# Performance work log

Measured on AMD Instinct MI355X. Metric: run time of the kernel, lower is better.

Reference implementation:

```python
import jax, jax.numpy as jnp
import numpy as np

DIM = 512
HEADS = 1
DIM_HEAD = DIM // 8          # 64
M = DIM // 2                 # 256 landmarks
ITERS = 6                    # pinv iterations
SCALE = DIM_HEAD ** -0.5
KSIZE = 33                   # residual conv kernel (seq dim)
EPS_LN = 1e-5


def setup_inputs() -> dict:
    key = jax.random.key(0)
    ks = jax.random.split(key, 6)
    B, N = 4, 4096  # N multiple of M -> no padding branch
    return {
        "x": jax.random.normal(ks[0], (B, N, DIM), jnp.float32),
        "norm_gamma": jnp.ones((DIM,), jnp.float32),
        "norm_beta": jnp.zeros((DIM,), jnp.float32),
        "w_qkv": jax.random.normal(ks[1], (DIM, 3 * HEADS * DIM_HEAD), jnp.float32) * 0.02,
        "w_out": jax.random.normal(ks[2], (HEADS * DIM_HEAD, DIM), jnp.float32) * 0.02,
        "b_out": jnp.zeros((DIM,), jnp.float32),
        "w_conv": jax.random.normal(ks[3], (HEADS, 1, KSIZE, 1), jnp.float32) * 0.02,
    }


def _moore_penrose_pinv(x, iters=ITERS):
    # x: [B, H, M, M]
    abs_x = jnp.abs(x)
    col = abs_x.sum(-1)
    row = abs_x.sum(-2)
    z = jnp.swapaxes(x, -1, -2) / (jnp.max(col) * jnp.max(row))  # global maxes, as in torch
    I = jnp.eye(x.shape[-1], dtype=x.dtype)
    for _ in range(iters):
        xz = x @ z
        z = 0.25 * z @ (13.0 * I - xz @ (15.0 * I - xz @ (7.0 * I - xz)))
    return z


def reference(x, norm_gamma, norm_beta, w_qkv, w_out, b_out, w_conv):
    B, N, _ = x.shape
    # LayerNorm (biased variance, matches torch)
    mu = x.mean(-1, keepdims=True)
    var = x.var(-1, keepdims=True)
    xn = (x - mu) / jnp.sqrt(var + EPS_LN) * norm_gamma + norm_beta

    qkv = xn @ w_qkv  # [B, N, 3*H*D]
    q, k, v = jnp.split(qkv, 3, axis=-1)
    resh = lambda t: t.reshape(B, N, HEADS, DIM_HEAD).transpose(0, 2, 1, 3)  # [B,H,N,D]
    q, k, v = resh(q), resh(k), resh(v)
    q = q * SCALE

    # landmarks: mean of l=N/M consecutive tokens
    l = N // M
    q_l = q.reshape(B, HEADS, M, l, DIM_HEAD).sum(3) / l  # [B,H,M,D]
    k_l = k.reshape(B, HEADS, M, l, DIM_HEAD).sum(3) / l

    sim1 = jnp.einsum('bhnd,bhmd->bhnm', q, k_l)    # [B,H,N,M]
    sim2 = jnp.einsum('bhid,bhjd->bhij', q_l, k_l)  # [B,H,M,M]
    sim3 = jnp.einsum('bhmd,bhnd->bhmn', q_l, k)    # [B,H,M,N]
    a1 = jax.nn.softmax(sim1, axis=-1)
    a2 = jax.nn.softmax(sim2, axis=-1)
    a3 = jax.nn.softmax(sim3, axis=-1)

    a2_inv = _moore_penrose_pinv(a2)
    left = a1 @ a2_inv                      # [B,H,N,M]
    out = left @ (a3 @ v)                   # [B,H,N,D]

    # residual depthwise conv over the sequence dim (treat [N,D] as HxW image)
    res = jax.lax.conv_general_dilated(
        v, w_conv, window_strides=(1, 1),
        padding=((KSIZE // 2, KSIZE // 2), (0, 0)),
        dimension_numbers=('NCHW', 'OIHW', 'NCHW'),
        feature_group_count=HEADS)
    out = out + res

    out = out.transpose(0, 2, 1, 3).reshape(B, N, HEADS * DIM_HEAD)
    out = out @ w_out + b_out               # to_out (dropout is eval no-op)

    attn = left @ a3                        # full approx attention [B,H,N,N]
    return (x + out, attn)
```

## Files before the change

kernel.cpp:

```cpp
#include <hip/hip_runtime.h>
#include <hip/hip_bf16.h>


typedef _Float16 f16;
typedef f16 f16x2 __attribute__((ext_vector_type(2)));
typedef f16 f16x4 __attribute__((ext_vector_type(4)));
typedef f16 f16x8 __attribute__((ext_vector_type(8)));
typedef float f32x4 __attribute__((ext_vector_type(4)));

__device__ __forceinline__ float waveMax(float v){
  #pragma unroll
  for(int i=32;i>0;i>>=1) v = fmaxf(v, __shfl_xor(v, i));
  return v;
}
__device__ __forceinline__ float waveSum(float v){
  #pragma unroll
  for(int i=32;i>0;i>>=1) v += __shfl_xor(v, i);
  return v;
}
__device__ __forceinline__ float blockMaxF(float v, float* sm){
  v = waveMax(v);
  if((threadIdx.x&63)==0) sm[threadIdx.x>>6] = v;
  __syncthreads();
  v = fmaxf(fmaxf(sm[0],sm[1]), fmaxf(sm[2],sm[3]));
  __syncthreads();
  return v;
}
__device__ __forceinline__ float blockSumF(float v, float* sm){
  v = waveSum(v);
  if((threadIdx.x&63)==0) sm[threadIdx.x>>6] = v;
  __syncthreads();
  v = sm[0]+sm[1]+sm[2]+sm[3];
  __syncthreads();
  return v;
}

__device__ __forceinline__ void st_out(float* p, float v){ *p = v; }
__device__ __forceinline__ void st_out(f16* p, float v){ *p = (f16)v; }

__device__ __forceinline__ void async_cp16(const f16* g, const f16* l){
  __builtin_amdgcn_global_load_lds((const __attribute__((address_space(1))) void*)g,
                                   (__attribute__((address_space(3))) void*)l, 16, 0, 0);
}

__global__ __launch_bounds__(256) void k_ln(const float* __restrict__ x, const float* __restrict__ g,
                                            const float* __restrict__ be, f16* __restrict__ xn){
  __shared__ float sm[8];
  long row = blockIdx.x; int t = threadIdx.x;
  const float* xr = x + row*512;
  float v0 = xr[t], v1 = xr[t+256];
  float s = waveSum(v0+v1), ss = waveSum(v0*v0+v1*v1);
  if((t&63)==0){ sm[t>>6] = s; sm[(t>>6)+4] = ss; }
  __syncthreads();
  s = sm[0]+sm[1]+sm[2]+sm[3]; ss = sm[4]+sm[5]+sm[6]+sm[7];
  float mu = s*(1.f/512.f);
  float var = ss*(1.f/512.f) - mu*mu;
  float rstd = rsqrtf(var + 1e-5f);
  xn[row*512+t]     = (f16)((v0-mu)*rstd*g[t]     + be[t]);
  xn[row*512+t+256] = (f16)((v1-mu)*rstd*g[t+256] + be[t+256]);
}

__global__ __launch_bounds__(256) void k_prep(const float* __restrict__ wqkv, const float* __restrict__ wout,
    f16* __restrict__ wqkT, f16* __restrict__ woutT, float* __restrict__ rs, unsigned* __restrict__ csmax){
  int blk = blockIdx.x, t = threadIdx.x;
  if(blk < 512){
    int i = blk*256 + t; int n = i>>9, k = i&511;
    wqkT[i] = (n<192) ? (f16)wqkv[k*192+n] : (f16)0.0f;
  } else if(blk < 640){
    int i = (blk-512)*256 + t; int n = i>>6, k = i&63;
    woutT[i] = (f16)wout[k*512+n];
  } else {
    rs[t]=0.f; rs[t+256]=0.f; rs[t+512]=0.f; rs[t+768]=0.f;
    if(t==0) *csmax = 0u;
  }
}

template<typename OutT>
__global__ __launch_bounds__(256) void gemm_bt(
    const f16* __restrict__ A, const f16* __restrict__ Bt, OutT* __restrict__ C,
    int M, int N, int K, long sA, long sB, long sC, int kbeg, int kend, int kslog,
    long sSlice, const float* __restrict__ bias, const float* __restrict__ resid)
{
  __shared__ f16 As[8192];
  __shared__ f16 Bs[8192];
  int zz = blockIdx.z;
  int b  = zz >> kslog;
  int ksl = zz & ((1<<kslog)-1);
  A  += (long)b * sA;  Bt += (long)b * sB;  C += (long)b * sC + (long)ksl * sSlice;
  int m0 = blockIdx.x*128, n0 = blockIdx.y*128;
  int t = threadIdx.x;
  int w = t>>6, lane = t&63;
  int quad = lane>>4, l16 = lane&15;
  int wr = w>>1, wc = w&1;
  int tiles = (kend - kbeg) >> 6;
  int per = tiles >> kslog;
  int kt0 = (kbeg>>6) + ksl*per;
  f32x4 acc[4][4] = {};
  for(int kt=kt0; kt<kt0+per; ++kt){
    #pragma unroll
    for(int i=0;i<4;++i){
      int G = (w<<8)+(i<<6)+lane;
      int row = G>>3, gs = G&7;
      int g = gs ^ (row&7);
      int koff = (kt<<6)+(g<<3);
      const f16* ldst = As + (((w<<8)+(i<<6))<<3);
      async_cp16(A + (long)(m0+row)*K + koff, ldst);
      const f16* ldst2 = Bs + (((w<<8)+(i<<6))<<3);
      async_cp16(Bt + (long)(n0+row)*K + koff, ldst2);
    }
    __syncthreads();
    #pragma unroll
    for(int kk=0; kk<2; ++kk){
      f16x8 af[4], bfr[4];
      int gb = (kk<<2) + quad;
      #pragma unroll
      for(int mi=0;mi<4;++mi){
        int row = (wr<<6)+(mi<<4)+l16;
        af[mi] = *(const f16x8*)(As + ((row<<6) + ((gb ^ (row&7))<<3)));
      }
      #pragma unroll
      for(int ni=0;ni<4;++ni){
        int row = (wc<<6)+(ni<<4)+l16;
        bfr[ni] = *(const f16x8*)(Bs + ((row<<6) + ((gb ^ (row&7))<<3)));
      }
      #pragma unroll
      for(int mi=0;mi<4;++mi){
        #pragma unroll
        for(int ni=0;ni<4;++ni)
          acc[mi][ni] = __builtin_amdgcn_mfma_f32_16x16x32_f16(af[mi], bfr[ni], acc[mi][ni], 0,0,0);
      }
    }
    __syncthreads();
  }
  #pragma unroll
  for(int mi=0;mi<4;++mi){
    int rowb = m0 + (wr<<6) + (mi<<4) + (quad<<2);
    #pragma unroll
    for(int ni=0;ni<4;++ni){
      int col = n0 + (wc<<6) + (ni<<4) + l16;
      if(col < N){
        #pragma unroll
        for(int r=0;r<4;++r){
          float v = acc[mi][ni][r];
          if(bias)  v += bias[col];
          if(resid) v += resid[(long)(rowb+r)*N + col];
          st_out(C + (long)(rowb+r)*N + col, v);
        }
      }
    }
  }
}

__global__ __launch_bounds__(256) void k_split(const float* __restrict__ qkv,
    f16* __restrict__ qf, f16* __restrict__ kf, float* __restrict__ vf){
  int t = threadIdx.x;
  long row = (long)blockIdx.x*4 + (t>>6); int d = t&63;
  const float* p = qkv + row*192;
  qf[row*64+d] = (f16)(p[d]*0.125f);
  kf[row*64+d] = (f16)(p[d+64]);
  vf[row*64+d] = p[d+128];
}

__global__ __launch_bounds__(256) void k_vT(const float* __restrict__ vf, f16* __restrict__ vT){
  __shared__ float tile[64][65];
  int b = blockIdx.y, n0 = blockIdx.x*64;
  int t = threadIdx.x; int c = t&63, r4 = t>>6;
  #pragma unroll
  for(int i=0;i<16;++i){ int r = i*4+r4; tile[r][c] = vf[((long)(b*4096 + n0 + r))*64 + c]; }
  __syncthreads();
  #pragma unroll
  for(int i=0;i<16;++i){ int d = i*4+r4;
    vT[((long)(b*128 + d))*4096 + n0 + c] = (f16)tile[c][d]; }
}

__global__ __launch_bounds__(256) void k_land(const f16* __restrict__ qf, const f16* __restrict__ kf,
                                              f16* __restrict__ ql, f16* __restrict__ kl){
  int t = threadIdx.x;
  int bm = blockIdx.x*4 + (t>>6); int d = t&63;
  const f16* pq = qf + (long)bm*1024 + d;
  const f16* pk = kf + (long)bm*1024 + d;
  float sq=0.f, sk=0.f;
  #pragma unroll
  for(int i=0;i<16;++i){ sq += (float)pq[i*64]; sk += (float)pk[i*64]; }
  ql[bm*64+d] = (f16)(sq*0.0625f);
  kl[bm*64+d] = (f16)(sk*0.0625f);
}

__global__ __launch_bounds__(256) void k_softmax1(const float* __restrict__ s, f16* __restrict__ a){
  int t = threadIdx.x; int w = t>>6, lane = t&63;
  long row = (long)blockIdx.x*4 + w;
  float4 v = *(const float4*)(s + row*256 + lane*4);
  float m = waveMax(fmaxf(fmaxf(v.x,v.y),fmaxf(v.z,v.w)));
  float e0 = __expf(v.x-m), e1 = __expf(v.y-m), e2 = __expf(v.z-m), e3 = __expf(v.w-m);
  float inv = 1.f/waveSum(e0+e1+e2+e3);
  f16x4 o = {(f16)(e0*inv),(f16)(e1*inv),(f16)(e2*inv),(f16)(e3*inv)};
  *(f16x4*)(a + row*256 + lane*4) = o;
}

__global__ __launch_bounds__(256) void k_softmax2(const float* __restrict__ s, float* __restrict__ a2,
                                                  float* __restrict__ rs, unsigned* __restrict__ csmax){
  __shared__ float sm[4];
  int row = blockIdx.x; int t = threadIdx.x; int b = row>>8;
  float v = s[row*256+t];
  float m = blockMaxF(v, sm);
  float e = __expf(v-m);
  float sum = blockSumF(e, sm);
  float p = e/sum;
  a2[(long)row*256+t] = p;
  atomicAdd(&rs[b*256+t], p);
  float rowsum = blockSumF(p, sm);
  if(t==0) atomicMax(csmax, __float_as_uint(rowsum));
}

__global__ __launch_bounds__(256) void k_softmax3(const float* __restrict__ s, f16* __restrict__ a){
  __shared__ float sm[4];
  long row = blockIdx.x; int t = threadIdx.x;
  const float* p = s + row*4096;
  float4 v[4]; float m = -1e30f;
  #pragma unroll
  for(int i=0;i<4;++i){
    v[i] = *(const float4*)(p + (i*256+t)*4);
    m = fmaxf(m, fmaxf(fmaxf(v[i].x,v[i].y),fmaxf(v[i].z,v[i].w)));
  }
  m = blockMaxF(m, sm);
  float sum = 0.f;
  #pragma unroll
  for(int i=0;i<4;++i){
    v[i].x = __expf(v[i].x-m); v[i].y = __expf(v[i].y-m);
    v[i].z = __expf(v[i].z-m); v[i].w = __expf(v[i].w-m);
    sum += v[i].x+v[i].y+v[i].z+v[i].w;
  }
  float inv = 1.f/blockSumF(sum, sm);
  f16* o = a + row*4096;
  #pragma unroll
  for(int i=0;i<4;++i){
    f16x4 ov = {(f16)(v[i].x*inv),(f16)(v[i].y*inv),(f16)(v[i].z*inv),(f16)(v[i].w*inv)};
    *(f16x4*)(o + (i*256+t)*4) = ov;
  }
}

__global__ __launch_bounds__(256) void k_z0(const float* __restrict__ a2, const float* __restrict__ rs,
                                            const unsigned* __restrict__ csmax, float* __restrict__ z){
  __shared__ float tile[64][65];
  __shared__ float sm[4];
  int b = blockIdx.z; int i0 = blockIdx.x*64, j0 = blockIdx.y*64;
  int t = threadIdx.x;
  float m = fmaxf(fmaxf(rs[t],rs[t+256]), fmaxf(rs[t+512],rs[t+768]));
  m = blockMaxF(m, sm);
  float sc = 1.f/(__uint_as_float(*csmax)*m);
  const float* A = a2 + (long)b*65536; float* Z = z + (long)b*65536;
  int c = t&63, r4 = t>>6;
  #pragma unroll
  for(int i=0;i<16;++i){ int r = i*4+r4; tile[r][c] = A[(j0+r)*256 + i0 + c]; }
  __syncthreads();
  #pragma unroll
  for(int i=0;i<16;++i){ int r = i*4+r4; Z[(i0+r)*256 + j0 + c] = tile[c][r]*sc; }
}

template<int AS, int BS, int ES>
__global__ __launch_bounds__(256) void gemm256s(const float* __restrict__ A, const float* __restrict__ B,
    const float* __restrict__ E, float* __restrict__ D, int Ncols, float beta, float alpha){
  __shared__ float At[16][72];
  __shared__ float Bs[16][72];
  int z = blockIdx.z; int b = z&3, ks = z>>2;
  long aOff = (long)b*65536;
  long bBatch = 256L*Ncols, bSl = 4L*bBatch;
  long bOff = (long)b*bBatch;
  long dOff = (long)ks*bSl + bOff;
  int r0 = blockIdx.x*64, c0 = blockIdx.y*64;
  int t = threadIdx.x, tr = t>>4, tc = t&15;
  int arow = t>>2, ac4 = t&3;
  int bk = t>>4, bn4 = t&15;
  float acc[4][4] = {};
  for(int k0=ks*64;k0<ks*64+64;k0+=16){
    const float* pa = A + aOff + (long)(r0+arow)*256 + k0 + ac4*4;
    float4 va = *(const float4*)pa;
    #pragma unroll
    for(int s=1;s<AS;++s){ float4 w = *(const float4*)(pa + (long)s*262144);
      va.x+=w.x; va.y+=w.y; va.z+=w.z; va.w+=w.w; }
    At[ac4*4+0][arow]=va.x; At[ac4*4+1][arow]=va.y; At[ac4*4+2][arow]=va.z; At[ac4*4+3][arow]=va.w;
    const float* pb = B + bOff + (long)(k0+bk)*Ncols + c0 + bn4*4;
    float4 vb = *(const float4*)pb;
    #pragma unroll
    for(int s=1;s<BS;++s){ float4 w = *(const float4*)(pb + (long)s*bSl);
      vb.x+=w.x; vb.y+=w.y; vb.z+=w.z; vb.w+=w.w; }
    *(float4*)&Bs[bk][bn4*4] = vb;
    __syncthreads();
    #pragma unroll
    for(int kk=0;kk<16;++kk){
      float4 a4 = *(const float4*)&At[kk][tr*4];
      float4 b4 = *(const float4*)&Bs[kk][tc*4];
      float av[4] = {a4.x,a4.y,a4.z,a4.w};
      float bv[4] = {b4.x,b4.y,b4.z,b4.w};
      #pragma unroll
      for(int i=0;i<4;++i){
        #pragma unroll
        for(int j=0;j<4;++j) acc[i][j] += av[i]*bv[j];
      }
    }
    __syncthreads();
  }
  #pragma unroll
  for(int i=0;i<4;++i){
    int row = r0 + tr*4 + i;
    #pragma unroll
    for(int j=0;j<4;++j){
      int col = c0 + tc*4 + j;
      float v = beta*acc[i][j];
      if(ES>0 && ks==0){
        const float* pe = E + aOff + (long)row*256 + col;
        float e = pe[0];
        #pragma unroll
        for(int s=1;s<ES;++s) e += pe[(long)s*262144];
        v += alpha*e;
      }
      D[dOff + (long)row*Ncols + col] = v;
    }
  }
}

__global__ __launch_bounds__(256) void k_zb(const float* __restrict__ z, f16* __restrict__ zb){
  int i = blockIdx.x*256 + threadIdx.x;
  float v = z[i] + z[i+262144] + z[i+524288] + z[i+786432];
  zb[i] = (f16)v;
}

__global__ __launch_bounds__(256) void k_trA3(const f16* __restrict__ a3, f16* __restrict__ a3T){
  __shared__ f16 tile[64][74];
  int b = blockIdx.z; int n0 = blockIdx.x*64, m0 = blockIdx.y*64;
  const f16* A = a3 + (long)b*1048576; f16* T = a3T + (long)b*1048576;
  int t = threadIdx.x; int c = t&63, r4 = t>>6;
  #pragma unroll
  for(int i=0;i<16;++i){ int r = i*4+r4; tile[r][c] = A[(long)(m0+r)*4096 + n0 + c]; }
  __syncthreads();
  #pragma unroll
  for(int i=0;i<16;++i){ int nr = i*4+r4; T[(long)(n0+nr)*256 + m0 + c] = tile[c][nr]; }
}

__global__ __launch_bounds__(256) void k_trZ(const float* __restrict__ pW, f16* __restrict__ zaT){
  int i = blockIdx.x*256 + threadIdx.x;
  int b = i>>15, j = i&32767; int d = j>>8, m = j&255;
  float v = 0.f;
  if(d<64){
    long base = (long)b*16384 + (long)m*64 + d;
    v = pW[base] + pW[base+65536] + pW[base+131072] + pW[base+196608];
  }
  zaT[i] = (f16)v;
}

__global__ __launch_bounds__(256) void k_h(const float* __restrict__ outh, const float* __restrict__ vf,
                                           const float* __restrict__ wconv, f16* __restrict__ h){
  __shared__ float wc[33];
  if(threadIdx.x<33) wc[threadIdx.x]=wconv[threadIdx.x];
  __syncthreads();
  long e = (long)blockIdx.x*256 + threadIdx.x;
  int d = (int)(e&63); long row = e>>6; int n = (int)(row&4095); long brow = row - n;
  float acc = outh[e];
  #pragma unroll
  for(int tau=0;tau<33;++tau){
    int nn = n + tau - 16;
    if(nn>=0 && nn<4096) acc += wc[tau]*vf[(brow+nn)*64 + d];
  }
  h[e] = (f16)acc;
}

extern "C" void kernel_launch(void* const* d_in, const int* in_sizes, int n_in,
                              void* d_out, int out_size, void* d_ws, size_t ws_size,
                              hipStream_t stream) {
  (void)in_sizes; (void)n_in; (void)out_size; (void)ws_size;
  const float* x     = (const float*)d_in[0];
  const float* gamma = (const float*)d_in[1];
  const float* beta  = (const float*)d_in[2];
  const float* wqkv  = (const float*)d_in[3];
  const float* wout  = (const float*)d_in[4];
  const float* bout  = (const float*)d_in[5];
  const float* wconv = (const float*)d_in[6];

  char* ws = (char*)d_ws;
  f16*   xn   = (f16*)(ws + 0);
  float* s3   = (float*)(ws + 0);
  float* s1   = (float*)(ws + 16777216);
  f16*   a3T  = (f16*)(ws + 16777216);
  f16*   U    = (f16*)(ws + 25165824);
  float* qkv  = (float*)(ws + 33554432);
  f16*   a3   = (f16*)(ws + 33554432);
  f16*   a1   = (f16*)(ws + 46137344);
  f16*   qf   = (f16*)(ws + 54525952);
  f16*   kf   = (f16*)(ws + 56623104);
  float* vf   = (float*)(ws + 58720256);
  f16*   vT   = (f16*)(ws + 62914560);
  f16*   wqkT = (f16*)(ws + 67108864);
  f16*   ql   = (f16*)(ws + 67371008);
  f16*   kl   = (f16*)(ws + 67502080);
  float* s2   = (float*)(ws + 67633152);
  float* a2   = (float*)(ws + 68681728);
  float* zA   = (float*)(ws + 69730304);
  f16*   zb   = (f16*)(ws + 74973184);
  float* rs   = (float*)(ws + 76021760);
  unsigned* csmax = (unsigned*)(ws + 76021760 + 4096);
  f16*   zaT  = (f16*)(ws + 76029952);
  f16*   woutT= (f16*)(ws + 76292096);
  float* outh = (float*)(ws + 76357632);
  f16*   h    = (f16*)(ws + 80551936);
  float* pXZ  = (float*)(ws + 82649088);
  float* pT1  = (float*)(ws + 86843392);
  float* pT2  = (float*)(ws + 91037696);
  float* pU0  = (float*)(ws + 95232000);
  float* pU1  = (float*)(ws + 99426304);
  float* a3vp = (float*)(ws + 103620608);
  float* pW   = (float*)(ws + 105717760);

  float* out0 = (float*)d_out;
  float* attn = out0 + 8388608;

  k_prep<<<641,256,0,stream>>>(wqkv, wout, wqkT, woutT, rs, csmax);
  k_ln<<<16384,256,0,stream>>>(x, gamma, beta, xn);
  gemm_bt<float><<<dim3(128,2,1),256,0,stream>>>(xn, wqkT, qkv, 16384,192,512, 0L,0L,0L, 0,512,0, 0L, nullptr,nullptr);
  k_split<<<4096,256,0,stream>>>(qkv, qf, kf, vf);
  k_vT<<<dim3(64,4),256,0,stream>>>(vf, vT);
  k_land<<<256,256,0,stream>>>(qf, kf, ql, kl);
  gemm_bt<float><<<dim3(32,2,4),256,0,stream>>>(qf, kl, s1, 4096,256,64, 262144L,16384L,1048576L, 0,64,0, 0L, nullptr,nullptr);
  gemm_bt<float><<<dim3(2,2,4),256,0,stream>>>(ql, kl, s2, 256,256,64, 16384L,16384L,65536L, 0,64,0, 0L, nullptr,nullptr);
  gemm_bt<float><<<dim3(2,32,4),256,0,stream>>>(ql, kf, s3, 256,4096,64, 16384L,262144L,1048576L, 0,64,0, 0L, nullptr,nullptr);
  k_softmax1<<<4096,256,0,stream>>>(s1, a1);
  k_softmax2<<<1024,256,0,stream>>>(s2, a2, rs, csmax);
  k_softmax3<<<1024,256,0,stream>>>(s3, a3);
  k_z0<<<dim3(4,4,4),256,0,stream>>>(a2, rs, csmax, zA);
  {
    float* cur = zA;
    float* bufs[2] = {pU0, pU1};
    for(int it=0; it<6; ++it){
      float* nxt = bufs[it&1];
      if(it==0) gemm256s<1,1,0><<<dim3(4,4,16),256,0,stream>>>(a2, cur, nullptr, pXZ, 256, 1.f, 0.f);
      else      gemm256s<1,4,0><<<dim3(4,4,16),256,0,stream>>>(a2, cur, nullptr, pXZ, 256, 1.f, 0.f);
      gemm256s<4,4,4><<<dim3(4,4,16),256,0,stream>>>(pXZ, pXZ, pXZ, pT1, 256, -1.f, 7.f);
      gemm256s<4,4,4><<<dim3(4,4,16),256,0,stream>>>(pXZ, pT1, pXZ, pT2, 256, -1.f, 15.f);
      if(it==0) gemm256s<1,4,1><<<dim3(4,4,16),256,0,stream>>>(cur, pT2, cur, nxt, 256, -0.25f, 3.25f);
      else      gemm256s<4,4,4><<<dim3(4,4,16),256,0,stream>>>(cur, pT2, cur, nxt, 256, -0.25f, 3.25f);
      cur = nxt;
    }
    k_zb<<<1024,256,0,stream>>>(cur, zb);
    k_trA3<<<dim3(64,4,4),256,0,stream>>>(a3, a3T);
    gemm_bt<float><<<dim3(2,1,32),256,0,stream>>>(a3, vT, a3vp, 256,64,4096, 1048576L,524288L,16384L, 0,4096,3, 65536L, nullptr,nullptr);
    gemm256s<4,8,0><<<dim3(4,1,16),256,0,stream>>>(cur, a3vp, nullptr, pW, 64, 1.f, 0.f);
  }
  k_trZ<<<512,256,0,stream>>>(pW, zaT);
  gemm_bt<float><<<dim3(32,1,4),256,0,stream>>>(a1, zaT, outh, 4096,64,256, 1048576L,32768L,262144L, 0,256,0, 0L, nullptr,nullptr);
  k_h<<<4096,256,0,stream>>>(outh, vf, wconv, h);
  gemm_bt<float><<<dim3(128,4,1),256,0,stream>>>(h, woutT, out0, 16384,512,64, 0L,0L,0L, 0,64,0, 0L, bout, x);
  gemm_bt<f16><<<dim3(32,2,4),256,0,stream>>>(a3T, zb, U, 4096,256,256, 1048576L,65536L,1048576L, 0,256,0, 0L, nullptr,nullptr);
  gemm_bt<float><<<dim3(32,32,4),256,0,stream>>>(a1, U, attn, 4096,4096,256, 1048576L,1048576L,16777216L, 0,256,0, 0L, nullptr,nullptr);
}
```

Measured before the change: 834.0 us.

## Merge independent stages into fused launches and run pinv loop in persistent kernel

Independent kernels are merged into multi-role launches that dispatch on block index: LN with weight prep, split with vT and landmarks, the three sim GEMMs, the three softmaxes, the outh and U GEMMs, and the out-projection with the attn GEMM. The 24 Newton-Schulz pinv GEMM launches plus z0, zb and trZ become one persistent 256-block kernel that uses a global atomic grid barrier between steps. The aim is to cut launch count and tail idle time between small kernels. The grid barrier assumes all 256 blocks are co-resident, and a spin-wait costs something of its own.

Result: slower. 1.389 ms (+66.5%).

```diff
diff --git a/kernel.cpp b/kernel.cpp
--- a/kernel.cpp
+++ b/kernel.cpp
@@ -35,78 +35,45 @@
   return v;
 }
 
-__device__ __forceinline__ void st_out(float* p, float v){ *p = v; }
-__device__ __forceinline__ void st_out(f16* p, float v){ *p = (f16)v; }
-
 __device__ __forceinline__ void async_cp16(const f16* g, const f16* l){
   __builtin_amdgcn_global_load_lds((const __attribute__((address_space(1))) void*)g,
                                    (__attribute__((address_space(3))) void*)l, 16, 0, 0);
 }
 
-__global__ __launch_bounds__(256) void k_ln(const float* __restrict__ x, const float* __restrict__ g,
-                                            const float* __restrict__ be, f16* __restrict__ xn){
-  __shared__ float sm[8];
-  long row = blockIdx.x; int t = threadIdx.x;
-  const float* xr = x + row*512;
-  float v0 = xr[t], v1 = xr[t+256];
-  float s = waveSum(v0+v1), ss = waveSum(v0*v0+v1*v1);
-  if((t&63)==0){ sm[t>>6] = s; sm[(t>>6)+4] = ss; }
-  __syncthreads();
-  s = sm[0]+sm[1]+sm[2]+sm[3]; ss = sm[4]+sm[5]+sm[6]+sm[7];
-  float mu = s*(1.f/512.f);
-  float var = ss*(1.f/512.f) - mu*mu;
-  float rstd = rsqrtf(var + 1e-5f);
-  xn[row*512+t]     = (f16)((v0-mu)*rstd*g[t]     + be[t]);
-  xn[row*512+t+256] = (f16)((v1-mu)*rstd*g[t+256] + be[t+256]);
-}
-
-__global__ __launch_bounds__(256) void k_prep(const float* __restrict__ wqkv, const float* __restrict__ wout,
-    f16* __restrict__ wqkT, f16* __restrict__ woutT, float* __restrict__ rs, unsigned* __restrict__ csmax){
-  int blk = blockIdx.x, t = threadIdx.x;
-  if(blk < 512){
-    int i = blk*256 + t; int n = i>>9, k = i&511;
-    wqkT[i] = (n<192) ? (f16)wqkv[k*192+n] : (f16)0.0f;
-  } else if(blk < 640){
-    int i = (blk-512)*256 + t; int n = i>>6, k = i&63;
-    woutT[i] = (f16)wout[k*512+n];
-  } else {
-    rs[t]=0.f; rs[t+256]=0.f; rs[t+512]=0.f; rs[t+768]=0.f;
-    if(t==0) *csmax = 0u;
-  }
-}
-
-template<typename OutT>
-__global__ __launch_bounds__(256) void gemm_bt(
-    const f16* __restrict__ A, const f16* __restrict__ Bt, OutT* __restrict__ C,
-    int M, int N, int K, long sA, long sB, long sC, int kbeg, int kend, int kslog,
-    long sSlice, const float* __restrict__ bias, const float* __restrict__ resid)
+__device__ __forceinline__ void gridBar(unsigned* bar, unsigned* s, int nb){
+  __syncthreads();
+  if(threadIdx.x==0){
+    __builtin_amdgcn_fence(__ATOMIC_RELEASE, "agent");
+    __hip_atomic_fetch_add(bar, 1u, __ATOMIC_RELAXED, __HIP_MEMORY_SCOPE_AGENT);
+    unsigned target = (unsigned)nb * (*s + 1u);
+    while(__hip_atomic_load(bar, __ATOMIC_RELAXED, __HIP_MEMORY_SCOPE_AGENT) < target)
+      __builtin_amdgcn_s_sleep(2);
+    __builtin_amdgcn_fence(__ATOMIC_ACQUIRE, "agent");
+  }
+  ++*s;
+  __syncthreads();
+}
+
+__device__ __forceinline__ void gemm_body(
+    const f16* __restrict__ A, const f16* __restrict__ Bt, void* __restrict__ C, int cf16,
+    int N, int K, int m0, int n0, int kt0, int ktn,
+    const float* __restrict__ bias, const float* __restrict__ resid,
+    f16* As, f16* Bs)
 {
-  __shared__ f16 As[8192];
-  __shared__ f16 Bs[8192];
-  int zz = blockIdx.z;
-  int b  = zz >> kslog;
-  int ksl = zz & ((1<<kslog)-1);
-  A  += (long)b * sA;  Bt += (long)b * sB;  C += (long)b * sC + (long)ksl * sSlice;
-  int m0 = blockIdx.x*128, n0 = blockIdx.y*128;
   int t = threadIdx.x;
   int w = t>>6, lane = t&63;
   int quad = lane>>4, l16 = lane&15;
   int wr = w>>1, wc = w&1;
-  int tiles = (kend - kbeg) >> 6;
-  int per = tiles >> kslog;
-  int kt0 = (kbeg>>6) + ksl*per;
   f32x4 acc[4][4] = {};
-  for(int kt=kt0; kt<kt0+per; ++kt){
+  for(int kt=kt0; kt<kt0+ktn; ++kt){
     #pragma unroll
     for(int i=0;i<4;++i){
       int G = (w<<8)+(i<<6)+lane;
       int row = G>>3, gs = G&7;
       int g = gs ^ (row&7);
       int koff = (kt<<6)+(g<<3);
-      const f16* ldst = As + (((w<<8)+(i<<6))<<3);
-      async_cp16(A + (long)(m0+row)*K + koff, ldst);
-      const f16* ldst2 = Bs + (((w<<8)+(i<<6))<<3);
-      async_cp16(Bt + (long)(n0+row)*K + koff, ldst2);
+      async_cp16(A + (long)(m0+row)*K + koff, As + (((w<<8)+(i<<6))<<3));
+      async_cp16(Bt + (long)(n0+row)*K + koff, Bs + (((w<<8)+(i<<6))<<3));
     }
     __syncthreads();
     #pragma unroll
@@ -144,130 +111,23 @@
           float v = acc[mi][ni][r];
           if(bias)  v += bias[col];
           if(resid) v += resid[(long)(rowb+r)*N + col];
-          st_out(C + (long)(rowb+r)*N + col, v);
+          if(cf16) ((f16*)C)[(long)(rowb+r)*N + col] = (f16)v;
+          else     ((float*)C)[(long)(rowb+r)*N + col] = v;
         }
       }
     }
   }
 }
 
-__global__ __launch_bounds__(256) void k_split(const float* __restrict__ qkv,
-    f16* __restrict__ qf, f16* __restrict__ kf, float* __restrict__ vf){
-  int t = threadIdx.x;
-  long row = (long)blockIdx.x*4 + (t>>6); int d = t&63;
-  const float* p = qkv + row*192;
-  qf[row*64+d] = (f16)(p[d]*0.125f);
-  kf[row*64+d] = (f16)(p[d+64]);
-  vf[row*64+d] = p[d+128];
-}
-
-__global__ __launch_bounds__(256) void k_vT(const float* __restrict__ vf, f16* __restrict__ vT){
-  __shared__ float tile[64][65];
-  int b = blockIdx.y, n0 = blockIdx.x*64;
-  int t = threadIdx.x; int c = t&63, r4 = t>>6;
-  #pragma unroll
-  for(int i=0;i<16;++i){ int r = i*4+r4; tile[r][c] = vf[((long)(b*4096 + n0 + r))*64 + c]; }
-  __syncthreads();
-  #pragma unroll
-  for(int i=0;i<16;++i){ int d = i*4+r4;
-    vT[((long)(b*128 + d))*4096 + n0 + c] = (f16)tile[c][d]; }
-}
-
-__global__ __launch_bounds__(256) void k_land(const f16* __restrict__ qf, const f16* __restrict__ kf,
-                                              f16* __restrict__ ql, f16* __restrict__ kl){
-  int t = threadIdx.x;
-  int bm = blockIdx.x*4 + (t>>6); int d = t&63;
-  const f16* pq = qf + (long)bm*1024 + d;
-  const f16* pk = kf + (long)bm*1024 + d;
-  float sq=0.f, sk=0.f;
-  #pragma unroll
-  for(int i=0;i<16;++i){ sq += (float)pq[i*64]; sk += (float)pk[i*64]; }
-  ql[bm*64+d] = (f16)(sq*0.0625f);
-  kl[bm*64+d] = (f16)(sk*0.0625f);
-}
-
-__global__ __launch_bounds__(256) void k_softmax1(const float* __restrict__ s, f16* __restrict__ a){
-  int t = threadIdx.x; int w = t>>6, lane = t&63;
-  long row = (long)blockIdx.x*4 + w;
-  float4 v = *(const float4*)(s + row*256 + lane*4);
-  float m = waveMax(fmaxf(fmaxf(v.x,v.y),fmaxf(v.z,v.w)));
-  float e0 = __expf(v.x-m), e1 = __expf(v.y-m), e2 = __expf(v.z-m), e3 = __expf(v.w-m);
-  float inv = 1.f/waveSum(e0+e1+e2+e3);
-  f16x4 o = {(f16)(e0*inv),(f16)(e1*inv),(f16)(e2*inv),(f16)(e3*inv)};
-  *(f16x4*)(a + row*256 + lane*4) = o;
-}
-
-__global__ __launch_bounds__(256) void k_softmax2(const float* __restrict__ s, float* __restrict__ a2,
-                                                  float* __restrict__ rs, unsigned* __restrict__ csmax){
-  __shared__ float sm[4];
-  int row = blockIdx.x; int t = threadIdx.x; int b = row>>8;
-  float v = s[row*256+t];
-  float m = blockMaxF(v, sm);
-  float e = __expf(v-m);
-  float sum = blockSumF(e, sm);
-  float p = e/sum;
-  a2[(long)row*256+t] = p;
-  atomicAdd(&rs[b*256+t], p);
-  float rowsum = blockSumF(p, sm);
-  if(t==0) atomicMax(csmax, __float_as_uint(rowsum));
-}
-
-__global__ __launch_bounds__(256) void k_softmax3(const float* __restrict__ s, f16* __restrict__ a){
-  __shared__ float sm[4];
-  long row = blockIdx.x; int t = threadIdx.x;
-  const float* p = s + row*4096;
-  float4 v[4]; float m = -1e30f;
-  #pragma unroll
-  for(int i=0;i<4;++i){
-    v[i] = *(const float4*)(p + (i*256+t)*4);
-    m = fmaxf(m, fmaxf(fmaxf(v[i].x,v[i].y),fmaxf(v[i].z,v[i].w)));
-  }
-  m = blockMaxF(m, sm);
-  float sum = 0.f;
-  #pragma unroll
-  for(int i=0;i<4;++i){
-    v[i].x = __expf(v[i].x-m); v[i].y = __expf(v[i].y-m);
-    v[i].z = __expf(v[i].z-m); v[i].w = __expf(v[i].w-m);
-    sum += v[i].x+v[i].y+v[i].z+v[i].w;
-  }
-  float inv = 1.f/blockSumF(sum, sm);
-  f16* o = a + row*4096;
-  #pragma unroll
-  for(int i=0;i<4;++i){
-    f16x4 ov = {(f16)(v[i].x*inv),(f16)(v[i].y*inv),(f16)(v[i].z*inv),(f16)(v[i].w*inv)};
-    *(f16x4*)(o + (i*256+t)*4) = ov;
-  }
-}
-
-__global__ __launch_bounds__(256) void k_z0(const float* __restrict__ a2, const float* __restrict__ rs,
-                                            const unsigned* __restrict__ csmax, float* __restrict__ z){
-  __shared__ float tile[64][65];
-  __shared__ float sm[4];
-  int b = blockIdx.z; int i0 = blockIdx.x*64, j0 = blockIdx.y*64;
-  int t = threadIdx.x;
-  float m = fmaxf(fmaxf(rs[t],rs[t+256]), fmaxf(rs[t+512],rs[t+768]));
-  m = blockMaxF(m, sm);
-  float sc = 1.f/(__uint_as_float(*csmax)*m);
-  const float* A = a2 + (long)b*65536; float* Z = z + (long)b*65536;
-  int c = t&63, r4 = t>>6;
-  #pragma unroll
-  for(int i=0;i<16;++i){ int r = i*4+r4; tile[r][c] = A[(j0+r)*256 + i0 + c]; }
-  __syncthreads();
-  #pragma unroll
-  for(int i=0;i<16;++i){ int r = i*4+r4; Z[(i0+r)*256 + j0 + c] = tile[c][r]*sc; }
-}
-
-template<int AS, int BS, int ES>
-__global__ __launch_bounds__(256) void gemm256s(const float* __restrict__ A, const float* __restrict__ B,
-    const float* __restrict__ E, float* __restrict__ D, int Ncols, float beta, float alpha){
-  __shared__ float At[16][72];
-  __shared__ float Bs[16][72];
-  int z = blockIdx.z; int b = z&3, ks = z>>2;
+__device__ __forceinline__ void g256_body(const float* __restrict__ A, const float* __restrict__ B,
+    const float* __restrict__ E, float* __restrict__ D, int Ncols, float beta, float alpha,
+    int AS, int BS, int ES, int bx, int by, int b, int ks, float* At, float* Bss)
+{
   long aOff = (long)b*65536;
   long bBatch = 256L*Ncols, bSl = 4L*bBatch;
   long bOff = (long)b*bBatch;
   long dOff = (long)ks*bSl + bOff;
-  int r0 = blockIdx.x*64, c0 = blockIdx.y*64;
+  int r0 = bx*64, c0 = by*64;
   int t = threadIdx.x, tr = t>>4, tc = t&15;
   int arow = t>>2, ac4 = t&3;
   int bk = t>>4, bn4 = t&15;
@@ -275,21 +135,20 @@
   for(int k0=ks*64;k0<ks*64+64;k0+=16){
     const float* pa = A + aOff + (long)(r0+arow)*256 + k0 + ac4*4;
     float4 va = *(const float4*)pa;
-    #pragma unroll
-    for(int s=1;s<AS;++s){ float4 w = *(const float4*)(pa + (long)s*262144);
-      va.x+=w.x; va.y+=w.y; va.z+=w.z; va.w+=w.w; }
-    At[ac4*4+0][arow]=va.x; At[ac4*4+1][arow]=va.y; At[ac4*4+2][arow]=va.z; At[ac4*4+3][arow]=va.w;
+    for(int s=1;s<AS;++s){ float4 w2 = *(const float4*)(pa + (long)s*262144);
+      va.x+=w2.x; va.y+=w2.y; va.z+=w2.z; va.w+=w2.w; }
+    At[(ac4*4+0)*72+arow]=va.x; At[(ac4*4+1)*72+arow]=va.y;
+    At[(ac4*4+2)*72+arow]=va.z; At[(ac4*4+3)*72+arow]=va.w;
     const float* pb = B + bOff + (long)(k0+bk)*Ncols + c0 + bn4*4;
     float4 vb = *(const float4*)pb;
-    #pragma unroll
-    for(int s=1;s<BS;++s){ float4 w = *(const float4*)(pb + (long)s*bSl);
-      vb.x+=w.x; vb.y+=w.y; vb.z+=w.z; vb.w+=w.w; }
-    *(float4*)&Bs[bk][bn4*4] = vb;
+    for(int s=1;s<BS;++s){ float4 w2 = *(const float4*)(pb + (long)s*bSl);
+      vb.x+=w2.x; vb.y+=w2.y; vb.z+=w2.z; vb.w+=w2.w; }
+    *(float4*)&Bss[bk*72+bn4*4] = vb;
     __syncthreads();
     #pragma unroll
     for(int kk=0;kk<16;++kk){
-      float4 a4 = *(const float4*)&At[kk][tr*4];
-      float4 b4 = *(const float4*)&Bs[kk][tc*4];
+      float4 a4 = *(const float4*)&At[kk*72+tr*4];
+      float4 b4 = *(const float4*)&Bss[kk*72+tc*4];
       float av[4] = {a4.x,a4.y,a4.z,a4.w};
       float bv[4] = {b4.x,b4.y,b4.z,b4.w};
       #pragma unroll
@@ -310,7 +169,6 @@
       if(ES>0 && ks==0){
         const float* pe = E + aOff + (long)row*256 + col;
         float e = pe[0];
-        #pragma unroll
         for(int s=1;s<ES;++s) e += pe[(long)s*262144];
         v += alpha*e;
       }
@@ -319,33 +177,263 @@
   }
 }
 
-__global__ __launch_bounds__(256) void k_zb(const float* __restrict__ z, f16* __restrict__ zb){
-  int i = blockIdx.x*256 + threadIdx.x;
-  float v = z[i] + z[i+262144] + z[i+524288] + z[i+786432];
-  zb[i] = (f16)v;
-}
-
-__global__ __launch_bounds__(256) void k_trA3(const f16* __restrict__ a3, f16* __restrict__ a3T){
+__global__ __launch_bounds__(256) void k_ln_prep(const float* __restrict__ x, const float* __restrict__ g,
+    const float* __restrict__ be, f16* __restrict__ xn, const float* __restrict__ wqkv,
+    const float* __restrict__ wout, f16* __restrict__ wqkT, f16* __restrict__ woutT,
+    float* __restrict__ rs, unsigned* __restrict__ csmax, unsigned* __restrict__ bar){
+  __shared__ float sm[8];
+  int blk = blockIdx.x; int t = threadIdx.x;
+  if(blk < 16384){
+    long row = blk;
+    const float* xr = x + row*512;
+    float v0 = xr[t], v1 = xr[t+256];
+    float s = waveSum(v0+v1), ss = waveSum(v0*v0+v1*v1);
+    if((t&63)==0){ sm[t>>6] = s; sm[(t>>6)+4] = ss; }
+    __syncthreads();
+    s = sm[0]+sm[1]+sm[2]+sm[3]; ss = sm[4]+sm[5]+sm[6]+sm[7];
+    float mu = s*(1.f/512.f);
+    float var = ss*(1.f/512.f) - mu*mu;
+    float rstd = rsqrtf(var + 1e-5f);
+    xn[row*512+t]     = (f16)((v0-mu)*rstd*g[t]     + be[t]);
+    xn[row*512+t+256] = (f16)((v1-mu)*rstd*g[t+256] + be[t+256]);
+  } else if(blk < 16896){
+    int i = (blk-16384)*256 + t; int n = i>>9, k = i&511;
+    wqkT[i] = (n<192) ? (f16)wqkv[k*192+n] : (f16)0.0f;
+  } else if(blk < 17024){
+    int i = (blk-16896)*256 + t; int n = i>>6, k = i&63;
+    woutT[i] = (f16)wout[k*512+n];
+  } else {
+    rs[t]=0.f; rs[t+256]=0.f; rs[t+512]=0.f; rs[t+768]=0.f;
+    if(t==0){ *csmax = 0u; *bar = 0u; }
+  }
+}
+
+__global__ __launch_bounds__(256) void k_qkv(const f16* __restrict__ xn, const f16* __restrict__ wqkT,
+                                             float* __restrict__ qkv){
+  __shared__ f16 As[8192];
+  __shared__ f16 Bs[8192];
+  int blk = blockIdx.x;
+  int bx = blk&127, by = blk>>7;
+  gemm_body(xn, wqkT, qkv, 0, 192, 512, bx*128, by*128, 0, 8, nullptr, nullptr, As, Bs);
+}
+
+__global__ __launch_bounds__(256) void k_splitvl(const float* __restrict__ qkv,
+    f16* __restrict__ qf, f16* __restrict__ kf, float* __restrict__ vf,
+    f16* __restrict__ vT, f16* __restrict__ ql, f16* __restrict__ kl){
+  __shared__ float tile[64][65];
+  int blk = blockIdx.x; int t = threadIdx.x;
+  if(blk < 4096){
+    long row = (long)blk*4 + (t>>6); int d = t&63;
+    const float* p = qkv + row*192;
+    qf[row*64+d] = (f16)(p[d]*0.125f);
+    kf[row*64+d] = (f16)(p[d+64]);
+    vf[row*64+d] = p[d+128];
+  } else if(blk < 4352){
+    int bidx = blk-4096; int b = bidx>>6, n0 = (bidx&63)*64;
+    int c = t&63, r4 = t>>6;
+    #pragma unroll
+    for(int i=0;i<16;++i){ int r = i*4+r4;
+      tile[r][c] = qkv[((long)(b*4096 + n0 + r))*192 + 128 + c]; }
+    __syncthreads();
+    #pragma unroll
+    for(int i=0;i<16;++i){ int d = i*4+r4;
+      vT[((long)(b*128 + d))*4096 + n0 + c] = (f16)tile[c][d]; }
+  } else {
+    int bidx = blk-4352;
+    int bm = bidx*4 + (t>>6); int d = t&63;
+    const float* p = qkv + (long)bm*16*192;
+    float sq=0.f, sk=0.f;
+    #pragma unroll
+    for(int i=0;i<16;++i){ sq += p[i*192+d]; sk += p[i*192+64+d]; }
+    ql[bm*64+d] = (f16)(sq*0.0625f*0.125f);
+    kl[bm*64+d] = (f16)(sk*0.0625f);
+  }
+}
+
+__global__ __launch_bounds__(256) void k_sims(const f16* __restrict__ qf, const f16* __restrict__ kf,
+    const f16* __restrict__ ql, const f16* __restrict__ kl,
+    float* __restrict__ s1, float* __restrict__ s2, float* __restrict__ s3){
+  __shared__ f16 As[8192];
+  __shared__ f16 Bs[8192];
+  int blk = blockIdx.x;
+  if(blk < 256){
+    int bx = blk&31, by = (blk>>5)&1, b = blk>>6;
+    gemm_body(qf + (long)b*262144, kl + (long)b*16384, s1 + (long)b*1048576, 0,
+              256, 64, bx*128, by*128, 0, 1, nullptr, nullptr, As, Bs);
+  } else if(blk < 272){
+    int idx = blk-256;
+    int bx = idx&1, by = (idx>>1)&1, b = idx>>2;
+    gemm_body(ql + (long)b*16384, kl + (long)b*16384, s2 + (long)b*65536, 0,
+              256, 64, bx*128, by*128, 0, 1, nullptr, nullptr, As, Bs);
+  } else {
+    int idx = blk-272;
+    int bx = idx&1, by = (idx>>1)&31, b = idx>>6;
+    gemm_body(ql + (long)b*16384, kf + (long)b*262144, s3 + (long)b*1048576, 0,
+              4096, 64, bx*128, by*128, 0, 1, nullptr, nullptr, As, Bs);
+  }
+}
+
+__global__ __launch_bounds__(256) void k_softmaxes(const float* __restrict__ s1, f16* __restrict__ a1,
+    const float* __restrict__ s2, float* __restrict__ a2, float* __restrict__ rs, unsigned* __restrict__ csmax,
+    const float* __restrict__ s3, f16* __restrict__ a3){
+  __shared__ float sm[4];
+  int blk = blockIdx.x; int t = threadIdx.x;
+  if(blk < 4096){
+    int w = t>>6, lane = t&63;
+    long row = (long)blk*4 + w;
+    float4 v = *(const float4*)(s1 + row*256 + lane*4);
+    float m = waveMax(fmaxf(fmaxf(v.x,v.y),fmaxf(v.z,v.w)));
+    float e0 = __expf(v.x-m), e1 = __expf(v.y-m), e2 = __expf(v.z-m), e3 = __expf(v.w-m);
+    float inv = 1.f/waveSum(e0+e1+e2+e3);
+    f16x4 o = {(f16)(e0*inv),(f16)(e1*inv),(f16)(e2*inv),(f16)(e3*inv)};
+    *(f16x4*)(a1 + row*256 + lane*4) = o;
+  } else if(blk < 5120){
+    int row = blk-4096; int b = row>>8;
+    float v = s2[row*256+t];
+    float m = blockMaxF(v, sm);
+    float e = __expf(v-m);
+    float sum = blockSumF(e, sm);
+    float p = e/sum;
+    a2[(long)row*256+t] = p;
+    atomicAdd(&rs[b*256+t], p);
+    float rowsum = blockSumF(p, sm);
+    if(t==0) atomicMax(csmax, __float_as_uint(rowsum));
+  } else {
+    long row = blk-5120;
+    const float* p = s3 + row*4096;
+    float4 v[4]; float m = -1e30f;
+    #pragma unroll
+    for(int i=0;i<4;++i){
+      v[i] = *(const float4*)(p + (i*256+t)*4);
+      m = fmaxf(m, fmaxf(fmaxf(v[i].x,v[i].y),fmaxf(v[i].z,v[i].w)));
+    }
+    m = blockMaxF(m, sm);
+    float sum = 0.f;
+    #pragma unroll
+    for(int i=0;i<4;++i){
+      v[i].x = __expf(v[i].x-m); v[i].y = __expf(v[i].y-m);
+      v[i].z = __expf(v[i].z-m); v[i].w = __expf(v[i].w-m);
+      sum += v[i].x+v[i].y+v[i].z+v[i].w;
+    }
+    float inv = 1.f/blockSumF(sum, sm);
+    f16* o = a3 + row*4096;
+    #pragma unroll
+    for(int i=0;i<4;++i){
+      f16x4 ov = {(f16)(v[i].x*inv),(f16)(v[i].y*inv),(f16)(v[i].z*inv),(f16)(v[i].w*inv)};
+      *(f16x4*)(o + (i*256+t)*4) = ov;
+    }
+  }
+}
+
+__global__ __launch_bounds__(256) void k_trA3_a3v(const f16* __restrict__ a3, f16* __restrict__ a3T,
+    const f16* __restrict__ vT, float* __restrict__ a3vp){
+  __shared__ f16 As[8192];
+  __shared__ f16 Bs[8192];
   __shared__ f16 tile[64][74];
-  int b = blockIdx.z; int n0 = blockIdx.x*64, m0 = blockIdx.y*64;
-  const f16* A = a3 + (long)b*1048576; f16* T = a3T + (long)b*1048576;
-  int t = threadIdx.x; int c = t&63, r4 = t>>6;
+  int blk = blockIdx.x; int t = threadIdx.x;
+  if(blk < 1024){
+    int bx = blk&63, by = (blk>>6)&3, b = blk>>8;
+    int n0 = bx*64, m0 = by*64;
+    const f16* A = a3 + (long)b*1048576; f16* T = a3T + (long)b*1048576;
+    int c = t&63, r4 = t>>6;
+    #pragma unroll
+    for(int i=0;i<16;++i){ int r = i*4+r4; tile[r][c] = A[(long)(m0+r)*4096 + n0 + c]; }
+    __syncthreads();
+    #pragma unroll
+    for(int i=0;i<16;++i){ int nr = i*4+r4; T[(long)(n0+nr)*256 + m0 + c] = tile[c][nr]; }
+  } else {
+    int idx = blk-1024;
+    int bx = idx&1, zz = idx>>1;
+    int b = zz>>3, ksl = zz&7;
+    gemm_body(a3 + (long)b*1048576, vT + (long)b*524288,
+              a3vp + (long)ksl*65536 + (long)b*16384, 0,
+              64, 4096, bx*128, 0, ksl*8, 8, nullptr, nullptr, As, Bs);
+  }
+}
+
+__global__ __launch_bounds__(256) void k_pinv(const float* __restrict__ a2, const float* __restrict__ rs,
+    const unsigned* __restrict__ csmax, float* __restrict__ zA,
+    float* __restrict__ pXZ, float* __restrict__ pT1, float* __restrict__ pT2,
+    float* __restrict__ pU0, float* __restrict__ pU1,
+    const float* __restrict__ a3vp, float* __restrict__ pW,
+    f16* __restrict__ zb, f16* __restrict__ zaT, unsigned* __restrict__ bar)
+{
+  __shared__ float smem[4164];
+  int blk = blockIdx.x; int t = threadIdx.x;
+  unsigned s = 0;
+  if(blk < 64){
+    int ix = blk&3, jy = (blk>>2)&3, b = blk>>4;
+    int i0 = ix*64, j0 = jy*64;
+    float m = fmaxf(fmaxf(rs[t],rs[t+256]), fmaxf(rs[t+512],rs[t+768]));
+    m = blockMaxF(m, smem+4160);
+    float sc = 1.f/(__uint_as_float(*csmax)*m);
+    const float* A = a2 + (long)b*65536; float* Z = zA + (long)b*65536;
+    int c = t&63, r4 = t>>6;
+    #pragma unroll
+    for(int i=0;i<16;++i){ int r = i*4+r4; smem[r*65+c] = A[(j0+r)*256 + i0 + c]; }
+    __syncthreads();
+    #pragma unroll
+    for(int i=0;i<16;++i){ int r = i*4+r4; Z[(i0+r)*256 + j0 + c] = smem[c*65+r]*sc; }
+  }
+  gridBar(bar, &s, 256);
+  int bx = blk&3, by = (blk>>2)&3, b4 = (blk>>4)&3, ks = blk>>6;
+  float* At = smem; float* Bss = smem+1152;
+  const float* cur = zA; int curAS = 1;
+  float* bufs[2] = {pU0, pU1};
+  for(int it=0; it<6; ++it){
+    float* nxt = bufs[it&1];
+    g256_body(a2, cur, nullptr, pXZ, 256, 1.f, 0.f, 1, curAS, 0, bx,by,b4,ks, At,Bss);
+    gridBar(bar, &s, 256);
+    g256_body(pXZ, pXZ, pXZ, pT1, 256, -1.f, 7.f, 4,4,4, bx,by,b4,ks, At,Bss);
+    gridBar(bar, &s, 256);
+    g256_body(pXZ, pT1, pXZ, pT2, 256, -1.f, 15.f, 4,4,4, bx,by,b4,ks, At,Bss);
+    gridBar(bar, &s, 256);
+    g256_body(cur, pT2, cur, nxt, 256, -0.25f, 3.25f, curAS,4,curAS, bx,by,b4,ks, At,Bss);
+    gridBar(bar, &s, 256);
+    cur = nxt; curAS = 4;
+  }
+  if(blk < 64){
+    int zx = blk&3, zz = blk>>2;
+    int zb4 = zz&3, zks = zz>>2;
+    g256_body(cur, a3vp, nullptr, pW, 64, 1.f, 0.f, 4,8,0, zx,0,zb4,zks, At,Bss);
+  } else if(blk < 192){
+    int base = (blk-64)*2048;
+    #pragma unroll
+    for(int k=0;k<8;++k){
+      int i = base + k*256 + t;
+      float v = cur[i] + cur[i+262144] + cur[i+524288] + cur[i+786432];
+      zb[i] = (f16)v;
+    }
+  }
+  gridBar(bar, &s, 256);
   #pragma unroll
-  for(int i=0;i<16;++i){ int r = i*4+r4; tile[r][c] = A[(long)(m0+r)*4096 + n0 + c]; }
-  __syncthreads();
-  #pragma unroll
-  for(int i=0;i<16;++i){ int nr = i*4+r4; T[(long)(n0+nr)*256 + m0 + c] = tile[c][nr]; }
-}
-
-__global__ __launch_bounds__(256) void k_trZ(const float* __restrict__ pW, f16* __restrict__ zaT){
-  int i = blockIdx.x*256 + threadIdx.x;
-  int b = i>>15, j = i&32767; int d = j>>8, m = j&255;
-  float v = 0.f;
-  if(d<64){
-    long base = (long)b*16384 + (long)m*64 + d;
-    v = pW[base] + pW[base+65536] + pW[base+131072] + pW[base+196608];
-  }
-  zaT[i] = (f16)v;
+  for(int j=0;j<2;++j){
+    int i = blk*512 + j*256 + t;
+    int b = i>>15, j2 = i&32767; int d = j2>>8, m = j2&255;
+    float v = 0.f;
+    if(d<64){
+      long base = (long)b*16384 + (long)m*64 + d;
+      v = pW[base] + pW[base+65536] + pW[base+131072] + pW[base+196608];
+    }
+    zaT[i] = (f16)v;
+  }
+}
+
+__global__ __launch_bounds__(256) void k_outh_U(const f16* __restrict__ a1, const f16* __restrict__ zaT,
+    float* __restrict__ outh, const f16* __restrict__ a3T, const f16* __restrict__ zb, f16* __restrict__ U){
+  __shared__ f16 As[8192];
+  __shared__ f16 Bs[8192];
+  int blk = blockIdx.x;
+  if(blk < 128){
+    int bx = blk&31, b = blk>>5;
+    gemm_body(a1 + (long)b*1048576, zaT + (long)b*32768, outh + (long)b*262144, 0,
+              64, 256, bx*128, 0, 0, 4, nullptr, nullptr, As, Bs);
+  } else {
+    int idx = blk-128;
+    int bx = idx&31, by = (idx>>5)&1, b = idx>>6;
+    gemm_body(a3T + (long)b*1048576, zb + (long)b*65536, U + (long)b*1048576, 1,
+              256, 256, bx*128, by*128, 0, 4, nullptr, nullptr, As, Bs);
+  }
 }
 
 __global__ __launch_bounds__(256) void k_h(const float* __restrict__ outh, const float* __restrict__ vf,
@@ -362,6 +450,23 @@
     if(nn>=0 && nn<4096) acc += wc[tau]*vf[(brow+nn)*64 + d];
   }
   h[e] = (f16)acc;
+}
+
+__global__ __launch_bounds__(256) void k_out_attn(const f16* __restrict__ h, const f16* __restrict__ woutT,
+    const float* __restrict__ x, const float* __restrict__ bout, float* __restrict__ out0,
+    const f16* __restrict__ a1, const f16* __restrict__ U, float* __restrict__ attn){
+  __shared__ f16 As[8192];
+  __shared__ f16 Bs[8192];
+  int blk = blockIdx.x;
+  if(blk < 512){
+    int bx = blk&127, by = blk>>7;
+    gemm_body(h, woutT, out0, 0, 512, 64, bx*128, by*128, 0, 1, bout, x, As, Bs);
+  } else {
+    int idx = blk-512;
+    int bx = idx&31, by = (idx>>5)&31, b = idx>>10;
+    gemm_body(a1 + (long)b*1048576, U + (long)b*1048576, attn + (long)b*16777216, 0,
+              4096, 256, bx*128, by*128, 0, 4, nullptr, nullptr, As, Bs);
+  }
 }
 
 extern "C" void kernel_launch(void* const* d_in, const int* in_sizes, int n_in,
@@ -398,6 +503,7 @@
   f16*   zb   = (f16*)(ws + 74973184);
   float* rs   = (float*)(ws + 76021760);
   unsigned* csmax = (unsigned*)(ws + 76021760 + 4096);
+  unsigned* bar   = (unsigned*)(ws + 76021760 + 4160);
   f16*   zaT  = (f16*)(ws + 76029952);
   f16*   woutT= (f16*)(ws + 76292096);
   float* outh = (float*)(ws + 76357632);
@@ -413,41 +519,14 @@
   float* out0 = (float*)d_out;
   float* attn = out0 + 8388608;
 
-  k_prep<<<641,256,0,stream>>>(wqkv, wout, wqkT, woutT, rs, csmax);
-  k_ln<<<16384,256,0,stream>>>(x, gamma, beta, xn);
-  gemm_bt<float><<<dim3(128,2,1),256,0,stream>>>(xn, wqkT, qkv, 16384,192,512, 0L,0L,0L, 0,512,0, 0L, nullptr,nullptr);
-  k_split<<<4096,256,0,stream>>>(qkv, qf, kf, vf);
-  k_vT<<<dim3(64,4),256,0,stream>>>(vf, vT);
-  k_land<<<256,256,0,stream>>>(qf, kf, ql, kl);
-  gemm_bt<float><<<dim3(32,2,4),256,0,stream>>>(qf, kl, s1, 4096,256,64, 262144L,16384L,1048576L, 0,64,0, 0L, nullptr,nullptr);
-  gemm_bt<float><<<dim3(2,2,4),256,0,stream>>>(ql, kl, s2, 256,256,64, 16384L,16384L,65536L, 0,64,0, 0L, nullptr,nullptr);
-  gemm_bt<float><<<dim3(2,32,4),256,0,stream>>>(ql, kf, s3, 256,4096,64, 16384L,262144L,1048576L, 0,64,0, 0L, nullptr,nullptr);
-  k_softmax1<<<4096,256,0,stream>>>(s1, a1);
-  k_softmax2<<<1024,256,0,stream>>>(s2, a2, rs, csmax);
-  k_softmax3<<<1024,256,0,stream>>>(s3, a3);
-  k_z0<<<dim3(4,4,4),256,0,stream>>>(a2, rs, csmax, zA);
-  {
-    float* cur = zA;
-    float* bufs[2] = {pU0, pU1};
-    for(int it=0; it<6; ++it){
-      float* nxt = bufs[it&1];
-      if(it==0) gemm256s<1,1,0><<<dim3(4,4,16),256,0,stream>>>(a2, cur, nullptr, pXZ, 256, 1.f, 0.f);
-      else      gemm256s<1,4,0><<<dim3(4,4,16),256,0,stream>>>(a2, cur, nullptr, pXZ, 256, 1.f, 0.f);
-      gemm256s<4,4,4><<<dim3(4,4,16),256,0,stream>>>(pXZ, pXZ, pXZ, pT1, 256, -1.f, 7.f);
-      gemm256s<4,4,4><<<dim3(4,4,16),256,0,stream>>>(pXZ, pT1, pXZ, pT2, 256, -1.f, 15.f);
-      if(it==0) gemm256s<1,4,1><<<dim3(4,4,16),256,0,stream>>>(cur, pT2, cur, nxt, 256, -0.25f, 3.25f);
-      else      gemm256s<4,4,4><<<dim3(4,4,16),256,0,stream>>>(cur, pT2, cur, nxt, 256, -0.25f, 3.25f);
-      cur = nxt;
-    }
-    k_zb<<<1024,256,0,stream>>>(cur, zb);
-    k_trA3<<<dim3(64,4,4),256,0,stream>>>(a3, a3T);
-    gemm_bt<float><<<dim3(2,1,32),256,0,stream>>>(a3, vT, a3vp, 256,64,4096, 1048576L,524288L,16384L, 0,4096,3, 65536L, nullptr,nullptr);
-    gemm256s<4,8,0><<<dim3(4,1,16),256,0,stream>>>(cur, a3vp, nullptr, pW, 64, 1.f, 0.f);
-  }
-  k_trZ<<<512,256,0,stream>>>(pW, zaT);
-  gemm_bt<float><<<dim3(32,1,4),256,0,stream>>>(a1, zaT, outh, 4096,64,256, 1048576L,32768L,262144L, 0,256,0, 0L, nullptr,nullptr);
+  k_ln_prep<<<17025,256,0,stream>>>(x, gamma, beta, xn, wqkv, wout, wqkT, woutT, rs, csmax, bar);
+  k_qkv<<<256,256,0,stream>>>(xn, wqkT, qkv);
+  k_splitvl<<<4608,256,0,stream>>>(qkv, qf, kf, vf, vT, ql, kl);
+  k_sims<<<528,256,0,stream>>>(qf, kf, ql, kl, s1, s2, s3);
+  k_softmaxes<<<6144,256,0,stream>>>(s1, a1, s2, a2, rs, csmax, s3, a3);
+  k_trA3_a3v<<<1088,256,0,stream>>>(a3, a3T, vT, a3vp);
+  k_pinv<<<256,256,0,stream>>>(a2, rs, csmax, zA, pXZ, pT1, pT2, pU0, pU1, a3vp, pW, zb, zaT, bar);
+  k_outh_U<<<384,256,0,stream>>>(a1, zaT, outh, a3T, zb, U);
   k_h<<<4096,256,0,stream>>>(outh, vf, wconv, h);
-  gemm_bt<float><<<dim3(128,4,1),256,0,stream>>>(h, woutT, out0, 16384,512,64, 0L,0L,0L, 0,64,0, 0L, bout, x);
-  gemm_bt<f16><<<dim3(32,2,4),256,0,stream>>>(a3T, zb, U, 4096,256,256, 1048576L,65536L,1048576L, 0,256,0, 0L, nullptr,nullptr);
-  gemm_bt<float><<<dim3(32,32,4),256,0,stream>>>(a1, U, attn, 4096,4096,256, 1048576L,1048576L,16777216L, 0,256,0, 0L, nullptr,nullptr);
-}
+  k_out_attn<<<4608,256,0,stream>>>(h, woutT, x, bout, out0, a1, U, attn);
+}
```
